# Optimization experiments

Hardware: AMD Instinct MI355X
Metric: run time of the kernel (lower is better)

The kernel has to match this reference:

```python
import jax, jax.numpy as jnp
import numpy as np

N_NODES = 1_000_000
N_EDGES = 16_000_000


def setup_inputs() -> dict:
    key = jax.random.key(0)
    k_feat, k_norm, k_src, k_dst, k_w1, k_w2 = jax.random.split(key, 6)
    feat = jax.random.normal(k_feat, (N_NODES, 1), dtype=jnp.float32)
    norm = jax.random.uniform(k_norm, (N_NODES, 1), dtype=jnp.float32)
    src = jax.random.randint(k_src, (N_EDGES,), 0, N_NODES, dtype=jnp.int64 if jax.config.read('jax_enable_x64') else jnp.int32)
    dst = jax.random.randint(k_dst, (N_EDGES,), 0, N_NODES, dtype=jnp.int64 if jax.config.read('jax_enable_x64') else jnp.int32)
    # GCNLayer1: in_feats=1 -> out_feats=3; GCNLayer2: 3 -> 1 (hardcoded in GCNProtein)
    W1 = jax.random.normal(k_w1, (1, 3), dtype=jnp.float32) * (1.0 / np.sqrt(1.0))
    b1 = jnp.zeros((3,), dtype=jnp.float32)
    W2 = jax.random.normal(k_w2, (3, 1), dtype=jnp.float32) * (1.0 / np.sqrt(3.0))
    b2 = jnp.zeros((1,), dtype=jnp.float32)
    return {"feat": feat, "norm": norm, "src": src, "dst": dst,
            "W1": W1, "b1": b1, "W2": W2, "b2": b2}


def gcn_layer(src, dst, x, norm, W, b):
    # symmetric-normalized GCN message passing (DGL GraphConv semantics):
    # h = norm * x ; h = sum_{(u->v) in E} h[u] scattered to v ; h = norm * h ; h = h @ W + b ; relu
    h = x * norm                                   # [N, F]
    msgs = jnp.take(h, src, axis=0)                # [E, F] gather (irregular)
    agg = jax.ops.segment_sum(msgs, dst, num_segments=x.shape[0])  # [N, F] scatter-add
    h = agg * norm                                 # [N, F]
    h = h @ W + b                                  # tiny GEMM: F_in -> F_out
    return jax.nn.relu(h)


def reference(feat, norm, src, dst, W1, b1, W2, b2):
    h = gcn_layer(src, dst, feat, norm, W1, b1)    # [N, 3]
    h = gcn_layer(src, dst, h, norm, W2, b2)       # [N, 1]
    return h
```

## Files before the change

kernel.cpp:

```cpp
#include <hip/hip_runtime.h>

#define BSHIFT 10
#define BSZ (1 << BSHIFT)
#define NBMAX 1024
#define NBIN_BLOCKS 1024
#define PB 512
#define BATCH 8192


__global__ void k1b(const float* __restrict__ feat, const float* __restrict__ norm,
                    float* __restrict__ g1, int n) {
    int stride = gridDim.x * blockDim.x;
    for (int i = blockIdx.x * blockDim.x + threadIdx.x; i < n; i += stride)
        g1[i] = feat[i] * norm[i];
}

__global__ void k1_prep(const float* __restrict__ feat, const float* __restrict__ norm,
                        float* __restrict__ g1, float* __restrict__ agg1,
                        float* __restrict__ agg2, int n) {
    int stride = gridDim.x * blockDim.x;
    for (int i = blockIdx.x * blockDim.x + threadIdx.x; i < n; i += stride) {
        g1[i] = feat[i] * norm[i];
        agg1[i] = 0.0f;
        agg2[i] = 0.0f;
    }
}

__global__ void k3_mid(const float* __restrict__ agg1, const float* __restrict__ norm,
                       const float* __restrict__ W1, const float* __restrict__ b1,
                       const float* __restrict__ W2, float* __restrict__ t, int n) {
    float w10 = W1[0], w11 = W1[1], w12 = W1[2];
    float b10 = b1[0], b11 = b1[1], b12 = b1[2];
    float w20 = W2[0], w21 = W2[1], w22 = W2[2];
    int stride = gridDim.x * blockDim.x;
    for (int i = blockIdx.x * blockDim.x + threadIdx.x; i < n; i += stride) {
        float nv = norm[i];
        float s = agg1[i] * nv;
        float h0 = fmaxf(fmaf(s, w10, b10), 0.0f);
        float h1 = fmaxf(fmaf(s, w11, b11), 0.0f);
        float h2 = fmaxf(fmaf(s, w12, b12), 0.0f);
        t[i] = nv * (h0 * w20 + h1 * w21 + h2 * w22);
    }
}

__global__ void k5_out(const float* __restrict__ agg2, const float* __restrict__ norm,
                       const float* __restrict__ b2, float* __restrict__ out, int n) {
    float b = b2[0];
    int stride = gridDim.x * blockDim.x;
    for (int i = blockIdx.x * blockDim.x + threadIdx.x; i < n; i += stride)
        out[i] = fmaxf(agg2[i] * norm[i] + b, 0.0f);
}


__global__ void k_hist(const int* __restrict__ dst, int nE, int NB, int chunk,
                       int* __restrict__ counts) {
    extern __shared__ int lhist[];
    int t = threadIdx.x;
    for (int b = t; b < NB; b += blockDim.x) lhist[b] = 0;
    __syncthreads();
    int lo = blockIdx.x * chunk;
    int hi = min(lo + chunk, nE);
    int n4 = (hi - lo) >> 2;
    const int4* d4 = (const int4*)(dst + lo);
    for (int i = t; i < n4; i += blockDim.x) {
        int4 v = d4[i];
        atomicAdd(&lhist[v.x >> BSHIFT], 1);
        atomicAdd(&lhist[v.y >> BSHIFT], 1);
        atomicAdd(&lhist[v.z >> BSHIFT], 1);
        atomicAdd(&lhist[v.w >> BSHIFT], 1);
    }
    for (int i = lo + (n4 << 2) + t; i < hi; i += blockDim.x)
        atomicAdd(&lhist[dst[i] >> BSHIFT], 1);
    __syncthreads();
    for (int b = t; b < NB; b += blockDim.x)
        counts[(size_t)b * NBIN_BLOCKS + blockIdx.x] = lhist[b];
}

__global__ void k_bucketscan(const int* __restrict__ counts,
                             int* __restrict__ chunkpre, int* __restrict__ tot) {
    __shared__ int ssum[256];
    int b = blockIdx.x;
    int t = threadIdx.x;
    const int4* in4 = (const int4*)(counts + (size_t)b * NBIN_BLOCKS);
    int4 v = in4[t];
    int mysum = v.x + v.y + v.z + v.w;
    ssum[t] = mysum;
    __syncthreads();
    for (int ofs = 1; ofs < 256; ofs <<= 1) {
        int add = (t >= ofs) ? ssum[t - ofs] : 0;
        __syncthreads();
        ssum[t] += add;
        __syncthreads();
    }
    int excl = ssum[t] - mysum;
    int4 o;
    o.x = excl;
    o.y = excl + v.x;
    o.z = o.y + v.y;
    o.w = o.z + v.z;
    ((int4*)(chunkpre + (size_t)b * NBIN_BLOCKS))[t] = o;
    if (t == 255) tot[b] = ssum[255];
}

__global__ void k_exscan(const int* __restrict__ tot, int NB, int* __restrict__ base) {
    __shared__ int s[1024];
    int t = threadIdx.x;
    if (NB < 1024) {
        int v = (t < NB) ? tot[t] : 0;
        s[t] = v;
        __syncthreads();
        for (int ofs = 1; ofs < 1024; ofs <<= 1) {
            int add = (t >= ofs) ? s[t - ofs] : 0;
            __syncthreads();
            s[t] += add;
            __syncthreads();
        }
        if (t < NB) base[t] = s[t] - v;
        if (t == NB) base[NB] = s[NB - 1];
    } else if (t == 0) {
        int run = 0;
        for (int b = 0; b < NB; ++b) { base[b] = run; run += tot[b]; }
        base[NB] = run;
    }
}

__global__ void __launch_bounds__(PB)
k_place2(const int* __restrict__ src, const int* __restrict__ dst,
         int nE, int NB, int chunk,
         const int* __restrict__ chunkpre, const int* __restrict__ base,
         unsigned int* __restrict__ bpack) {
    __shared__ unsigned int spack[BATCH];
    __shared__ unsigned short sbkt[BATCH];
    __shared__ int lcur[NBMAX];
    __shared__ int loff[NBMAX + 1];
    __shared__ int gcur[NBMAX];
    __shared__ int ssc[PB];
    int t = threadIdx.x;
    int blk = blockIdx.x;

    for (int b = t; b < NB; b += PB)
        gcur[b] = base[b] + chunkpre[(size_t)b * NBIN_BLOCKS + blk];

    int lo = blk * chunk;
    int hi = min(lo + chunk, nE);
    for (int bs = lo; bs < hi; bs += BATCH) {
        int be = min(bs + BATCH, hi);
        int cnt = be - bs;
        lcur[2 * t] = 0;
        lcur[2 * t + 1] = 0;
        __syncthreads();
        int n4 = cnt >> 2;
        const int4* d4 = (const int4*)(dst + bs);
        for (int i = t; i < n4; i += PB) {
            int4 v = d4[i];
            atomicAdd(&lcur[v.x >> BSHIFT], 1);
            atomicAdd(&lcur[v.y >> BSHIFT], 1);
            atomicAdd(&lcur[v.z >> BSHIFT], 1);
            atomicAdd(&lcur[v.w >> BSHIFT], 1);
        }
        for (int i = bs + (n4 << 2) + t; i < be; i += PB)
            atomicAdd(&lcur[dst[i] >> BSHIFT], 1);
        __syncthreads();
        int a = lcur[2 * t];
        int c = lcur[2 * t + 1];
        int s = a + c;
        ssc[t] = s;
        __syncthreads();
        for (int ofs = 1; ofs < PB; ofs <<= 1) {
            int add = (t >= ofs) ? ssc[t - ofs] : 0;
            __syncthreads();
            ssc[t] += add;
            __syncthreads();
        }
        int excl = ssc[t] - s;
        loff[2 * t] = excl;
        loff[2 * t + 1] = excl + a;
        lcur[2 * t] = excl;
        lcur[2 * t + 1] = excl + a;
        if (t == PB - 1) loff[2 * PB] = ssc[PB - 1];
        __syncthreads();
        const int4* s4 = (const int4*)(src + bs);
        for (int i = t; i < n4; i += PB) {
            int4 dv = d4[i];
            int4 sv = s4[i];
            int b0 = dv.x >> BSHIFT, p0 = atomicAdd(&lcur[b0], 1);
            spack[p0] = ((unsigned int)sv.x << BSHIFT) | (unsigned int)(dv.x & (BSZ - 1));
            sbkt[p0] = (unsigned short)b0;
            int b1 = dv.y >> BSHIFT, p1 = atomicAdd(&lcur[b1], 1);
            spack[p1] = ((unsigned int)sv.y << BSHIFT) | (unsigned int)(dv.y & (BSZ - 1));
            sbkt[p1] = (unsigned short)b1;
            int b2 = dv.z >> BSHIFT, p2 = atomicAdd(&lcur[b2], 1);
            spack[p2] = ((unsigned int)sv.z << BSHIFT) | (unsigned int)(dv.z & (BSZ - 1));
            sbkt[p2] = (unsigned short)b2;
            int b3 = dv.w >> BSHIFT, p3 = atomicAdd(&lcur[b3], 1);
            spack[p3] = ((unsigned int)sv.w << BSHIFT) | (unsigned int)(dv.w & (BSZ - 1));
            sbkt[p3] = (unsigned short)b3;
        }
        for (int i = bs + (n4 << 2) + t; i < be; i += PB) {
            int d = dst[i];
            int b = d >> BSHIFT;
            int pos = atomicAdd(&lcur[b], 1);
            spack[pos] = ((unsigned int)src[i] << BSHIFT) | (unsigned int)(d & (BSZ - 1));
            sbkt[pos] = (unsigned short)b;
        }
        __syncthreads();
        for (int j = t; j < cnt; j += PB) {
            int b = sbkt[j];
            bpack[gcur[b] + (j - loff[b])] = spack[j];
        }
        __syncthreads();
        for (int b = t; b < NB; b += PB)
            gcur[b] += loff[b + 1] - loff[b];
        __syncthreads();
    }
}

__device__ __forceinline__ void acc_body(const unsigned int* __restrict__ bpack,
                                         int lo, int hi,
                                         const float* __restrict__ val,
                                         float* acc) {
    int head = min((4 - (lo & 3)) & 3, hi - lo);
    for (int i = lo + (int)threadIdx.x; i < lo + head; i += blockDim.x) {
        unsigned int w = bpack[i];
        atomicAdd(&acc[w & (BSZ - 1)], val[w >> BSHIFT]);
    }
    int lo4 = lo + head;
    int n4 = (hi - lo4) >> 2;
    const uint4* p4 = (const uint4*)(bpack + lo4);
    int i = threadIdx.x;
    int bd = blockDim.x;
    for (; i + bd < n4; i += 2 * bd) {
        uint4 wa = p4[i];
        uint4 wb = p4[i + bd];
        float va0 = val[wa.x >> BSHIFT], va1 = val[wa.y >> BSHIFT];
        float va2 = val[wa.z >> BSHIFT], va3 = val[wa.w >> BSHIFT];
        float vb0 = val[wb.x >> BSHIFT], vb1 = val[wb.y >> BSHIFT];
        float vb2 = val[wb.z >> BSHIFT], vb3 = val[wb.w >> BSHIFT];
        atomicAdd(&acc[wa.x & (BSZ - 1)], va0);
        atomicAdd(&acc[wa.y & (BSZ - 1)], va1);
        atomicAdd(&acc[wa.z & (BSZ - 1)], va2);
        atomicAdd(&acc[wa.w & (BSZ - 1)], va3);
        atomicAdd(&acc[wb.x & (BSZ - 1)], vb0);
        atomicAdd(&acc[wb.y & (BSZ - 1)], vb1);
        atomicAdd(&acc[wb.z & (BSZ - 1)], vb2);
        atomicAdd(&acc[wb.w & (BSZ - 1)], vb3);
    }
    for (; i < n4; i += bd) {
        uint4 w = p4[i];
        atomicAdd(&acc[w.x & (BSZ - 1)], val[w.x >> BSHIFT]);
        atomicAdd(&acc[w.y & (BSZ - 1)], val[w.y >> BSHIFT]);
        atomicAdd(&acc[w.z & (BSZ - 1)], val[w.z >> BSHIFT]);
        atomicAdd(&acc[w.w & (BSZ - 1)], val[w.w >> BSHIFT]);
    }
    for (int j = lo4 + (n4 << 2) + (int)threadIdx.x; j < hi; j += blockDim.x) {
        unsigned int w = bpack[j];
        atomicAdd(&acc[w & (BSZ - 1)], val[w >> BSHIFT]);
    }
}

__global__ void k_acc1(const unsigned int* __restrict__ bpack,
                       const int* __restrict__ base,
                       const float* __restrict__ val, const float* __restrict__ norm,
                       const float* __restrict__ W1, const float* __restrict__ b1,
                       const float* __restrict__ W2,
                       float* __restrict__ t, int nN) {
    __shared__ float acc[BSZ];
    for (int j = threadIdx.x; j < BSZ; j += blockDim.x) acc[j] = 0.0f;
    __syncthreads();
    int b = blockIdx.x;
    acc_body(bpack, base[b], base[b + 1], val, acc);
    __syncthreads();
    float w10 = W1[0], w11 = W1[1], w12 = W1[2];
    float b10 = b1[0], b11 = b1[1], b12 = b1[2];
    float w20 = W2[0], w21 = W2[1], w22 = W2[2];
    int node0 = b << BSHIFT;
    for (int j = threadIdx.x; j < BSZ && node0 + j < nN; j += blockDim.x) {
        float nv = norm[node0 + j];
        float s = acc[j] * nv;
        float h0 = fmaxf(fmaf(s, w10, b10), 0.0f);
        float h1 = fmaxf(fmaf(s, w11, b11), 0.0f);
        float h2 = fmaxf(fmaf(s, w12, b12), 0.0f);
        t[node0 + j] = nv * (h0 * w20 + h1 * w21 + h2 * w22);
    }
}

__global__ void k_acc2(const unsigned int* __restrict__ bpack,
                       const int* __restrict__ base,
                       const float* __restrict__ val, const float* __restrict__ norm,
                       const float* __restrict__ b2,
                       float* __restrict__ out, int nN) {
    __shared__ float acc[BSZ];
    for (int j = threadIdx.x; j < BSZ; j += blockDim.x) acc[j] = 0.0f;
    __syncthreads();
    int b = blockIdx.x;
    acc_body(bpack, base[b], base[b + 1], val, acc);
    __syncthreads();
    float bb = b2[0];
    int node0 = b << BSHIFT;
    for (int j = threadIdx.x; j < BSZ && node0 + j < nN; j += blockDim.x)
        out[node0 + j] = fmaxf(acc[j] * norm[node0 + j] + bb, 0.0f);
}

__global__ void k_edge_scatter(const int* __restrict__ src, const int* __restrict__ dst,
                               const float* __restrict__ val, float* __restrict__ agg,
                               int nE) {
    int stride = gridDim.x * blockDim.x;
    for (int e = blockIdx.x * blockDim.x + threadIdx.x; e < nE; e += stride)
        atomicAdd(&agg[dst[e]], val[src[e]]);
}

static inline size_t align256(size_t x) { return (x + 255) & ~(size_t)255; }

extern "C" void kernel_launch(void* const* d_in, const int* in_sizes, int n_in,
                              void* d_out, int out_size, void* d_ws, size_t ws_size,
                              hipStream_t stream) {
    const float* feat = (const float*)d_in[0];
    const float* norm = (const float*)d_in[1];
    const int*   src  = (const int*)d_in[2];
    const int*   dst  = (const int*)d_in[3];
    const float* W1   = (const float*)d_in[4];
    const float* b1   = (const float*)d_in[5];
    const float* W2   = (const float*)d_in[6];
    const float* b2   = (const float*)d_in[7];
    float* out = (float*)d_out;

    int nN = in_sizes[0];
    int nE = in_sizes[2];
    int NB = (nN + BSZ - 1) >> BSHIFT;

    char* p = (char*)d_ws;
    size_t off = 0;
    float* g1   = (float*)(p + off); off = align256(off + (size_t)nN * 4);
    float* agg1 = (float*)(p + off); off = align256(off + (size_t)nN * 4);
    int* base     = (int*)(p + off); off = align256(off + (size_t)(NB + 1) * 4);
    int* tot      = (int*)(p + off); off = align256(off + (size_t)NB * 4);
    float* agg2   = (float*)(p + off);
    int* counts   = (int*)(p + off); off = align256(off + (size_t)NB * NBIN_BLOCKS * 4);
    int* chunkpre = (int*)(p + off); off = align256(off + (size_t)NB * NBIN_BLOCKS * 4);
    unsigned int* bpack = (unsigned int*)(p + off); off = align256(off + (size_t)nE * 4);
    size_t need = off;

    const int BLK = 256;
    int nodeBlocks = (nN + BLK - 1) / BLK;
    if (nodeBlocks > 2048) nodeBlocks = 2048;

    bool packed_ok = ((size_t)nN <= ((size_t)1 << (32 - BSHIFT))) && (NB <= NBMAX);
    if (ws_size >= need && packed_ok) {
        int chunk = (nE + NBIN_BLOCKS - 1) / NBIN_BLOCKS;
        chunk = (chunk + 3) & ~3;
        size_t ldsNB = (size_t)NB * 4;

        k1b<<<nodeBlocks, BLK, 0, stream>>>(feat, norm, g1, nN);
        k_hist<<<NBIN_BLOCKS, 256, ldsNB, stream>>>(dst, nE, NB, chunk, counts);
        k_bucketscan<<<NB, 256, 0, stream>>>(counts, chunkpre, tot);
        k_exscan<<<1, 1024, 0, stream>>>(tot, NB, base);
        k_place2<<<NBIN_BLOCKS, PB, 0, stream>>>(src, dst, nE, NB, chunk,
                                                 chunkpre, base, bpack);
        k_acc1<<<NB, 512, 0, stream>>>(bpack, base, g1, norm, W1, b1, W2, agg1, nN);
        k_acc2<<<NB, 512, 0, stream>>>(bpack, base, agg1, norm, b2, out, nN);
    } else {
        int edgeBlocks = 2048;
        k1_prep<<<nodeBlocks, BLK, 0, stream>>>(feat, norm, g1, agg1, agg2, nN);
        k_edge_scatter<<<edgeBlocks, BLK, 0, stream>>>(src, dst, g1, agg1, nE);
        k3_mid<<<nodeBlocks, BLK, 0, stream>>>(agg1, norm, W1, b1, W2, g1, nN);
        k_edge_scatter<<<edgeBlocks, BLK, 0, stream>>>(src, dst, g1, agg2, nE);
        k5_out<<<nodeBlocks, BLK, 0, stream>>>(agg2, norm, b2, out, nN);
    }
}
```

Before: 282.7 us.

## Widen dst buckets to 2048 nodes and split each bucket across two blocks

Doubles the bucket width so there are about 489 buckets, which simplifies the per-batch scan in the placement kernel to one bucket per thread. Each bucket's edge range is then split between two accumulation blocks that write partial sums to global memory, and separate merge kernels add the two halves and apply the norm, weights and relu. This keeps the number of accumulation blocks near the old count while halving per-block LDS atomic contention ranges. The cost is extra global traffic for the partials, two more kernel launches, and twice the LDS accumulator per block. The histogram block size also grows to 512.

```diff
diff --git a/kernel.cpp b/kernel.cpp
--- a/kernel.cpp
+++ b/kernel.cpp
@@ -1,8 +1,8 @@
 #include <hip/hip_runtime.h>
 
-#define BSHIFT 10
+#define BSHIFT 11
 #define BSZ (1 << BSHIFT)
-#define NBMAX 1024
+#define NBMAX 512
 #define NBIN_BLOCKS 1024
 #define PB 512
 #define BATCH 8192
@@ -134,7 +134,7 @@
     __shared__ int lcur[NBMAX];
     __shared__ int loff[NBMAX + 1];
     __shared__ int gcur[NBMAX];
-    __shared__ int ssc[PB];
+    __shared__ int ssc[NBMAX];
     int t = threadIdx.x;
     int blk = blockIdx.x;
 
@@ -146,8 +146,7 @@
     for (int bs = lo; bs < hi; bs += BATCH) {
         int be = min(bs + BATCH, hi);
         int cnt = be - bs;
-        lcur[2 * t] = 0;
-        lcur[2 * t + 1] = 0;
+        lcur[t] = 0;
         __syncthreads();
         int n4 = cnt >> 2;
         const int4* d4 = (const int4*)(dst + bs);
@@ -161,23 +160,19 @@
         for (int i = bs + (n4 << 2) + t; i < be; i += PB)
             atomicAdd(&lcur[dst[i] >> BSHIFT], 1);
         __syncthreads();
-        int a = lcur[2 * t];
-        int c = lcur[2 * t + 1];
-        int s = a + c;
-        ssc[t] = s;
-        __syncthreads();
-        for (int ofs = 1; ofs < PB; ofs <<= 1) {
+        int v = lcur[t];
+        ssc[t] = v;
+        __syncthreads();
+        for (int ofs = 1; ofs < 512; ofs <<= 1) {
             int add = (t >= ofs) ? ssc[t - ofs] : 0;
             __syncthreads();
             ssc[t] += add;
             __syncthreads();
         }
-        int excl = ssc[t] - s;
-        loff[2 * t] = excl;
-        loff[2 * t + 1] = excl + a;
-        lcur[2 * t] = excl;
-        lcur[2 * t + 1] = excl + a;
-        if (t == PB - 1) loff[2 * PB] = ssc[PB - 1];
+        int excl = ssc[t] - v;
+        loff[t] = excl;
+        lcur[t] = excl;
+        if (t == 511) loff[512] = ssc[511];
         __syncthreads();
         const int4* s4 = (const int4*)(src + bs);
         for (int i = t; i < n4; i += PB) {
@@ -258,47 +253,64 @@
     }
 }
 
-__global__ void k_acc1(const unsigned int* __restrict__ bpack,
+__global__ void k_accp(const unsigned int* __restrict__ bpack,
                        const int* __restrict__ base,
-                       const float* __restrict__ val, const float* __restrict__ norm,
-                       const float* __restrict__ W1, const float* __restrict__ b1,
-                       const float* __restrict__ W2,
-                       float* __restrict__ t, int nN) {
+                       const float* __restrict__ val,
+                       float* __restrict__ partial, int nN) {
     __shared__ float acc[BSZ];
     for (int j = threadIdx.x; j < BSZ; j += blockDim.x) acc[j] = 0.0f;
     __syncthreads();
-    int b = blockIdx.x;
-    acc_body(bpack, base[b], base[b + 1], val, acc);
-    __syncthreads();
+    int bid = blockIdx.x;
+    int b = bid >> 1;
+    int s = bid & 1;
+    int lo = base[b], hi = base[b + 1];
+    int mid = (lo + hi) >> 1;
+    int rlo = s ? mid : lo;
+    int rhi = s ? hi : mid;
+    acc_body(bpack, rlo, rhi, val, acc);
+    __syncthreads();
+    float* dstp = partial + (size_t)s * nN;
+    int node0 = b << BSHIFT;
+    int lim = min(BSZ, nN - node0);
+    int l4 = lim >> 2;
+    float4* d4 = (float4*)(dstp + node0);
+    const float4* a4 = (const float4*)acc;
+    for (int j = threadIdx.x; j < l4; j += blockDim.x) d4[j] = a4[j];
+    for (int j = (l4 << 2) + (int)threadIdx.x; j < lim; j += blockDim.x)
+        dstp[node0 + j] = acc[j];
+}
+
+__global__ void k_merge1(const float* __restrict__ partial,
+                         const float* __restrict__ norm,
+                         const float* __restrict__ W1, const float* __restrict__ b1,
+                         const float* __restrict__ W2,
+                         float* __restrict__ t, int nN) {
     float w10 = W1[0], w11 = W1[1], w12 = W1[2];
     float b10 = b1[0], b11 = b1[1], b12 = b1[2];
     float w20 = W2[0], w21 = W2[1], w22 = W2[2];
-    int node0 = b << BSHIFT;
-    for (int j = threadIdx.x; j < BSZ && node0 + j < nN; j += blockDim.x) {
-        float nv = norm[node0 + j];
-        float s = acc[j] * nv;
+    const float* p0 = partial;
+    const float* p1 = partial + nN;
+    int stride = gridDim.x * blockDim.x;
+    for (int i = blockIdx.x * blockDim.x + threadIdx.x; i < nN; i += stride) {
+        float nv = norm[i];
+        float s = (p0[i] + p1[i]) * nv;
         float h0 = fmaxf(fmaf(s, w10, b10), 0.0f);
         float h1 = fmaxf(fmaf(s, w11, b11), 0.0f);
         float h2 = fmaxf(fmaf(s, w12, b12), 0.0f);
-        t[node0 + j] = nv * (h0 * w20 + h1 * w21 + h2 * w22);
-    }
-}
-
-__global__ void k_acc2(const unsigned int* __restrict__ bpack,
-                       const int* __restrict__ base,
-                       const float* __restrict__ val, const float* __restrict__ norm,
-                       const float* __restrict__ b2,
-                       float* __restrict__ out, int nN) {
-    __shared__ float acc[BSZ];
-    for (int j = threadIdx.x; j < BSZ; j += blockDim.x) acc[j] = 0.0f;
-    __syncthreads();
-    int b = blockIdx.x;
-    acc_body(bpack, base[b], base[b + 1], val, acc);
-    __syncthreads();
+        t[i] = nv * (h0 * w20 + h1 * w21 + h2 * w22);
+    }
+}
+
+__global__ void k_merge2(const float* __restrict__ partial,
+                         const float* __restrict__ norm,
+                         const float* __restrict__ b2,
+                         float* __restrict__ out, int nN) {
     float bb = b2[0];
-    int node0 = b << BSHIFT;
-    for (int j = threadIdx.x; j < BSZ && node0 + j < nN; j += blockDim.x)
-        out[node0 + j] = fmaxf(acc[j] * norm[node0 + j] + bb, 0.0f);
+    const float* p0 = partial;
+    const float* p1 = partial + nN;
+    int stride = gridDim.x * blockDim.x;
+    for (int i = blockIdx.x * blockDim.x + threadIdx.x; i < nN; i += stride)
+        out[i] = fmaxf((p0[i] + p1[i]) * norm[i] + bb, 0.0f);
 }
 
 __global__ void k_edge_scatter(const int* __restrict__ src, const int* __restrict__ dst,
@@ -332,6 +344,7 @@
     size_t off = 0;
     float* g1   = (float*)(p + off); off = align256(off + (size_t)nN * 4);
     float* agg1 = (float*)(p + off); off = align256(off + (size_t)nN * 4);
+    float* partial = (float*)(p + off); off = align256(off + 2 * (size_t)nN * 4);
     int* base     = (int*)(p + off); off = align256(off + (size_t)(NB + 1) * 4);
     int* tot      = (int*)(p + off); off = align256(off + (size_t)NB * 4);
     float* agg2   = (float*)(p + off);
@@ -351,13 +364,15 @@
         size_t ldsNB = (size_t)NB * 4;
 
         k1b<<<nodeBlocks, BLK, 0, stream>>>(feat, norm, g1, nN);
-        k_hist<<<NBIN_BLOCKS, 256, ldsNB, stream>>>(dst, nE, NB, chunk, counts);
+        k_hist<<<NBIN_BLOCKS, 512, ldsNB, stream>>>(dst, nE, NB, chunk, counts);
         k_bucketscan<<<NB, 256, 0, stream>>>(counts, chunkpre, tot);
         k_exscan<<<1, 1024, 0, stream>>>(tot, NB, base);
         k_place2<<<NBIN_BLOCKS, PB, 0, stream>>>(src, dst, nE, NB, chunk,
                                                  chunkpre, base, bpack);
-        k_acc1<<<NB, 512, 0, stream>>>(bpack, base, g1, norm, W1, b1, W2, agg1, nN);
-        k_acc2<<<NB, 512, 0, stream>>>(bpack, base, agg1, norm, b2, out, nN);
+        k_accp<<<2 * NB, 512, 0, stream>>>(bpack, base, g1, partial, nN);
+        k_merge1<<<nodeBlocks, BLK, 0, stream>>>(partial, norm, W1, b1, W2, agg1, nN);
+        k_accp<<<2 * NB, 512, 0, stream>>>(bpack, base, agg1, partial, nN);
+        k_merge2<<<nodeBlocks, BLK, 0, stream>>>(partial, norm, b2, out, nN);
     } else {
         int edgeBlocks = 2048;
         k1_prep<<<nodeBlocks, BLK, 0, stream>>>(feat, norm, g1, agg1, agg2, nN);
```

Result: faster. 274.6 us (-2.9%).

## Embed first-layer gathered values in bucketed edge records and widen buckets

Applied to the files above, without the earlier changes.

During the bucket-placement pass, each edge record now also carries g1[src], stored as an 8-byte (packed index, value) pair. The first accumulation kernel can then read values in a streaming fashion instead of doing random gathers. The bucket width doubles to 2048 nodes, so there are half as many bucket blocks, and loads and stores of the bucket array use nontemporal hints. The cost is twice the bpack write and read traffic, plus the random gather moving into the placement kernel. The second layer still gathers from the 8-byte records, reading unused value slots.

```diff
diff --git a/kernel.cpp b/kernel.cpp
--- a/kernel.cpp
+++ b/kernel.cpp
@@ -1,11 +1,15 @@
 #include <hip/hip_runtime.h>
 
-#define BSHIFT 10
+#define BSHIFT 11
 #define BSZ (1 << BSHIFT)
-#define NBMAX 1024
+#define NBMAX 512
 #define NBIN_BLOCKS 1024
 #define PB 512
 #define BATCH 8192
+
+typedef int          int32x4  __attribute__((ext_vector_type(4)));
+typedef unsigned int uint32x4 __attribute__((ext_vector_type(4)));
+typedef unsigned int uint32x2 __attribute__((ext_vector_type(2)));
 
 
 __global__ void k1b(const float* __restrict__ feat, const float* __restrict__ norm,
@@ -124,17 +128,18 @@
     }
 }
 
+template <bool IV>
 __global__ void __launch_bounds__(PB)
-k_place2(const int* __restrict__ src, const int* __restrict__ dst,
-         int nE, int NB, int chunk,
-         const int* __restrict__ chunkpre, const int* __restrict__ base,
-         unsigned int* __restrict__ bpack) {
+k_place2x(const int* __restrict__ src, const int* __restrict__ dst,
+          const float* __restrict__ g1, int nE, int NB, int chunk,
+          const int* __restrict__ chunkpre, const int* __restrict__ base,
+          unsigned int* __restrict__ bpack, uint32x2* __restrict__ bpack2) {
     __shared__ unsigned int spack[BATCH];
     __shared__ unsigned short sbkt[BATCH];
     __shared__ int lcur[NBMAX];
     __shared__ int loff[NBMAX + 1];
     __shared__ int gcur[NBMAX];
-    __shared__ int ssc[PB];
+    __shared__ int ssc[NBMAX];
     int t = threadIdx.x;
     int blk = blockIdx.x;
 
@@ -146,8 +151,7 @@
     for (int bs = lo; bs < hi; bs += BATCH) {
         int be = min(bs + BATCH, hi);
         int cnt = be - bs;
-        lcur[2 * t] = 0;
-        lcur[2 * t + 1] = 0;
+        lcur[t] = 0;
         __syncthreads();
         int n4 = cnt >> 2;
         const int4* d4 = (const int4*)(dst + bs);
@@ -161,23 +165,19 @@
         for (int i = bs + (n4 << 2) + t; i < be; i += PB)
             atomicAdd(&lcur[dst[i] >> BSHIFT], 1);
         __syncthreads();
-        int a = lcur[2 * t];
-        int c = lcur[2 * t + 1];
-        int s = a + c;
-        ssc[t] = s;
-        __syncthreads();
-        for (int ofs = 1; ofs < PB; ofs <<= 1) {
+        int v = lcur[t];
+        ssc[t] = v;
+        __syncthreads();
+        for (int ofs = 1; ofs < 512; ofs <<= 1) {
             int add = (t >= ofs) ? ssc[t - ofs] : 0;
             __syncthreads();
             ssc[t] += add;
             __syncthreads();
         }
-        int excl = ssc[t] - s;
-        loff[2 * t] = excl;
-        loff[2 * t + 1] = excl + a;
-        lcur[2 * t] = excl;
-        lcur[2 * t + 1] = excl + a;
-        if (t == PB - 1) loff[2 * PB] = ssc[PB - 1];
+        int excl = ssc[t] - v;
+        loff[t] = excl;
+        lcur[t] = excl;
+        if (t == 511) loff[512] = ssc[511];
         __syncthreads();
         const int4* s4 = (const int4*)(src + bs);
         for (int i = t; i < n4; i += PB) {
@@ -205,8 +205,18 @@
         }
         __syncthreads();
         for (int j = t; j < cnt; j += PB) {
+            unsigned int w = spack[j];
             int b = sbkt[j];
-            bpack[gcur[b] + (j - loff[b])] = spack[j];
+            int gi = gcur[b] + (j - loff[b]);
+            if (IV) {
+                float vv = g1[w >> BSHIFT];
+                uint32x2 o;
+                o[0] = w;
+                o[1] = __float_as_uint(vv);
+                __builtin_nontemporal_store(o, bpack2 + gi);
+            } else {
+                __builtin_nontemporal_store(w, bpack + gi);
+            }
         }
         __syncthreads();
         for (int b = t; b < NB; b += PB)
@@ -214,6 +224,105 @@
         __syncthreads();
     }
 }
+
+
+__global__ void k_acc1v2(const uint32x2* __restrict__ bp, const int* __restrict__ base,
+                         const float* __restrict__ norm,
+                         const float* __restrict__ W1, const float* __restrict__ b1,
+                         const float* __restrict__ W2,
+                         float* __restrict__ t, int nN) {
+    __shared__ float acc[BSZ];
+    for (int j = threadIdx.x; j < BSZ; j += blockDim.x) acc[j] = 0.0f;
+    __syncthreads();
+    int b = blockIdx.x;
+    int lo = base[b], hi = base[b + 1];
+    int head = ((lo & 1) && lo < hi) ? 1 : 0;
+    if (head && threadIdx.x == 0) {
+        uint32x2 w = bp[lo];
+        atomicAdd(&acc[w[0] & (BSZ - 1)], __uint_as_float(w[1]));
+    }
+    int lo2 = lo + head;
+    int n2 = (hi - lo2) >> 1;
+    const uint32x4* p4 = (const uint32x4*)(bp + lo2);
+    int i = threadIdx.x, bd = blockDim.x;
+    for (; i + bd < n2; i += 2 * bd) {
+        uint32x4 a = __builtin_nontemporal_load(p4 + i);
+        uint32x4 c = __builtin_nontemporal_load(p4 + i + bd);
+        atomicAdd(&acc[a[0] & (BSZ - 1)], __uint_as_float(a[1]));
+        atomicAdd(&acc[a[2] & (BSZ - 1)], __uint_as_float(a[3]));
+        atomicAdd(&acc[c[0] & (BSZ - 1)], __uint_as_float(c[1]));
+        atomicAdd(&acc[c[2] & (BSZ - 1)], __uint_as_float(c[3]));
+    }
+    for (; i < n2; i += bd) {
+        uint32x4 a = __builtin_nontemporal_load(p4 + i);
+        atomicAdd(&acc[a[0] & (BSZ - 1)], __uint_as_float(a[1]));
+        atomicAdd(&acc[a[2] & (BSZ - 1)], __uint_as_float(a[3]));
+    }
+    for (int j = lo2 + (n2 << 1) + (int)threadIdx.x; j < hi; j += bd) {
+        uint32x2 w = bp[j];
+        atomicAdd(&acc[w[0] & (BSZ - 1)], __uint_as_float(w[1]));
+    }
+    __syncthreads();
+    float w10 = W1[0], w11 = W1[1], w12 = W1[2];
+    float b10 = b1[0], b11 = b1[1], b12 = b1[2];
+    float w20 = W2[0], w21 = W2[1], w22 = W2[2];
+    int node0 = b << BSHIFT;
+    for (int j = threadIdx.x; j < BSZ && node0 + j < nN; j += blockDim.x) {
+        float nv = norm[node0 + j];
+        float s = acc[j] * nv;
+        float h0 = fmaxf(fmaf(s, w10, b10), 0.0f);
+        float h1 = fmaxf(fmaf(s, w11, b11), 0.0f);
+        float h2 = fmaxf(fmaf(s, w12, b12), 0.0f);
+        t[node0 + j] = nv * (h0 * w20 + h1 * w21 + h2 * w22);
+    }
+}
+
+__global__ void k_acc2v2(const uint32x2* __restrict__ bp, const int* __restrict__ base,
+                         const float* __restrict__ val, const float* __restrict__ norm,
+                         const float* __restrict__ b2,
+                         float* __restrict__ out, int nN) {
+    __shared__ float acc[BSZ];
+    for (int j = threadIdx.x; j < BSZ; j += blockDim.x) acc[j] = 0.0f;
+    __syncthreads();
+    int b = blockIdx.x;
+    int lo = base[b], hi = base[b + 1];
+    int head = ((lo & 1) && lo < hi) ? 1 : 0;
+    if (head && threadIdx.x == 0) {
+        uint32x2 w = bp[lo];
+        atomicAdd(&acc[w[0] & (BSZ - 1)], val[w[0] >> BSHIFT]);
+    }
+    int lo2 = lo + head;
+    int n2 = (hi - lo2) >> 1;
+    const uint32x4* p4 = (const uint32x4*)(bp + lo2);
+    int i = threadIdx.x, bd = blockDim.x;
+    for (; i + bd < n2; i += 2 * bd) {
+        uint32x4 a = __builtin_nontemporal_load(p4 + i);
+        uint32x4 c = __builtin_nontemporal_load(p4 + i + bd);
+        float v0 = val[a[0] >> BSHIFT];
+        float v1 = val[a[2] >> BSHIFT];
+        float v2 = val[c[0] >> BSHIFT];
+        float v3 = val[c[2] >> BSHIFT];
+        atomicAdd(&acc[a[0] & (BSZ - 1)], v0);
+        atomicAdd(&acc[a[2] & (BSZ - 1)], v1);
+        atomicAdd(&acc[c[0] & (BSZ - 1)], v2);
+        atomicAdd(&acc[c[2] & (BSZ - 1)], v3);
+    }
+    for (; i < n2; i += bd) {
+        uint32x4 a = __builtin_nontemporal_load(p4 + i);
+        atomicAdd(&acc[a[0] & (BSZ - 1)], val[a[0] >> BSHIFT]);
+        atomicAdd(&acc[a[2] & (BSZ - 1)], val[a[2] >> BSHIFT]);
+    }
+    for (int j = lo2 + (n2 << 1) + (int)threadIdx.x; j < hi; j += bd) {
+        uint32x2 w = bp[j];
+        atomicAdd(&acc[w[0] & (BSZ - 1)], val[w[0] >> BSHIFT]);
+    }
+    __syncthreads();
+    float bb = b2[0];
+    int node0 = b << BSHIFT;
+    for (int j = threadIdx.x; j < BSZ && node0 + j < nN; j += blockDim.x)
+        out[node0 + j] = fmaxf(acc[j] * norm[node0 + j] + bb, 0.0f);
+}
+
 
 __device__ __forceinline__ void acc_body(const unsigned int* __restrict__ bpack,
                                          int lo, int hi,
@@ -226,31 +335,31 @@
     }
     int lo4 = lo + head;
     int n4 = (hi - lo4) >> 2;
-    const uint4* p4 = (const uint4*)(bpack + lo4);
+    const uint32x4* p4 = (const uint32x4*)(bpack + lo4);
     int i = threadIdx.x;
     int bd = blockDim.x;
     for (; i + bd < n4; i += 2 * bd) {
-        uint4 wa = p4[i];
-        uint4 wb = p4[i + bd];
-        float va0 = val[wa.x >> BSHIFT], va1 = val[wa.y >> BSHIFT];
-        float va2 = val[wa.z >> BSHIFT], va3 = val[wa.w >> BSHIFT];
-        float vb0 = val[wb.x >> BSHIFT], vb1 = val[wb.y >> BSHIFT];
-        float vb2 = val[wb.z >> BSHIFT], vb3 = val[wb.w >> BSHIFT];
-        atomicAdd(&acc[wa.x & (BSZ - 1)], va0);
-        atomicAdd(&acc[wa.y & (BSZ - 1)], va1);
-        atomicAdd(&acc[wa.z & (BSZ - 1)], va2);
-        atomicAdd(&acc[wa.w & (BSZ - 1)], va3);
-        atomicAdd(&acc[wb.x & (BSZ - 1)], vb0);
-        atomicAdd(&acc[wb.y & (BSZ - 1)], vb1);
-        atomicAdd(&acc[wb.z & (BSZ - 1)], vb2);
-        atomicAdd(&acc[wb.w & (BSZ - 1)], vb3);
+        uint32x4 wa = __builtin_nontemporal_load(p4 + i);
+        uint32x4 wb = __builtin_nontemporal_load(p4 + i + bd);
+        float va0 = val[wa[0] >> BSHIFT], va1 = val[wa[1] >> BSHIFT];
+        float va2 = val[wa[2] >> BSHIFT], va3 = val[wa[3] >> BSHIFT];
+        float vb0 = val[wb[0] >> BSHIFT], vb1 = val[wb[1] >> BSHIFT];
+        float vb2 = val[wb[2] >> BSHIFT], vb3 = val[wb[3] >> BSHIFT];
+        atomicAdd(&acc[wa[0] & (BSZ - 1)], va0);
+        atomicAdd(&acc[wa[1] & (BSZ - 1)], va1);
+        atomicAdd(&acc[wa[2] & (BSZ - 1)], va2);
+        atomicAdd(&acc[wa[3] & (BSZ - 1)], va3);
+        atomicAdd(&acc[wb[0] & (BSZ - 1)], vb0);
+        atomicAdd(&acc[wb[1] & (BSZ - 1)], vb1);
+        atomicAdd(&acc[wb[2] & (BSZ - 1)], vb2);
+        atomicAdd(&acc[wb[3] & (BSZ - 1)], vb3);
     }
     for (; i < n4; i += bd) {
-        uint4 w = p4[i];
-        atomicAdd(&acc[w.x & (BSZ - 1)], val[w.x >> BSHIFT]);
-        atomicAdd(&acc[w.y & (BSZ - 1)], val[w.y >> BSHIFT]);
-        atomicAdd(&acc[w.z & (BSZ - 1)], val[w.z >> BSHIFT]);
-        atomicAdd(&acc[w.w & (BSZ - 1)], val[w.w >> BSHIFT]);
+        uint32x4 w = __builtin_nontemporal_load(p4 + i);
+        atomicAdd(&acc[w[0] & (BSZ - 1)], val[w[0] >> BSHIFT]);
+        atomicAdd(&acc[w[1] & (BSZ - 1)], val[w[1] >> BSHIFT]);
+        atomicAdd(&acc[w[2] & (BSZ - 1)], val[w[2] >> BSHIFT]);
+        atomicAdd(&acc[w[3] & (BSZ - 1)], val[w[3] >> BSHIFT]);
     }
     for (int j = lo4 + (n4 << 2) + (int)threadIdx.x; j < hi; j += blockDim.x) {
         unsigned int w = bpack[j];
@@ -330,39 +439,50 @@
 
     char* p = (char*)d_ws;
     size_t off = 0;
-    float* g1   = (float*)(p + off); off = align256(off + (size_t)nN * 4);
-    float* agg1 = (float*)(p + off); off = align256(off + (size_t)nN * 4);
+    float* g1 = (float*)(p + off); off = align256(off + (size_t)nN * 4);
+    float* t1 = (float*)(p + off); off = align256(off + (size_t)nN * 4);
     int* base     = (int*)(p + off); off = align256(off + (size_t)(NB + 1) * 4);
     int* tot      = (int*)(p + off); off = align256(off + (size_t)NB * 4);
     float* agg2   = (float*)(p + off);
     int* counts   = (int*)(p + off); off = align256(off + (size_t)NB * NBIN_BLOCKS * 4);
     int* chunkpre = (int*)(p + off); off = align256(off + (size_t)NB * NBIN_BLOCKS * 4);
-    unsigned int* bpack = (unsigned int*)(p + off); off = align256(off + (size_t)nE * 4);
-    size_t need = off;
+    size_t off_common = off;
+    uint32x2* bpack2 = (uint32x2*)(p + off_common);
+    unsigned int* bpack = (unsigned int*)(p + off_common);
+    size_t need2 = align256(off_common + (size_t)nE * 8);
+    size_t need1 = align256(off_common + (size_t)nE * 4);
 
     const int BLK = 256;
     int nodeBlocks = (nN + BLK - 1) / BLK;
     if (nodeBlocks > 2048) nodeBlocks = 2048;
 
     bool packed_ok = ((size_t)nN <= ((size_t)1 << (32 - BSHIFT))) && (NB <= NBMAX);
-    if (ws_size >= need && packed_ok) {
+    if (packed_ok && ws_size >= need1) {
         int chunk = (nE + NBIN_BLOCKS - 1) / NBIN_BLOCKS;
         chunk = (chunk + 3) & ~3;
         size_t ldsNB = (size_t)NB * 4;
+        bool v2 = (ws_size >= need2);
 
         k1b<<<nodeBlocks, BLK, 0, stream>>>(feat, norm, g1, nN);
-        k_hist<<<NBIN_BLOCKS, 256, ldsNB, stream>>>(dst, nE, NB, chunk, counts);
+        k_hist<<<NBIN_BLOCKS, 512, ldsNB, stream>>>(dst, nE, NB, chunk, counts);
         k_bucketscan<<<NB, 256, 0, stream>>>(counts, chunkpre, tot);
         k_exscan<<<1, 1024, 0, stream>>>(tot, NB, base);
-        k_place2<<<NBIN_BLOCKS, PB, 0, stream>>>(src, dst, nE, NB, chunk,
-                                                 chunkpre, base, bpack);
-        k_acc1<<<NB, 512, 0, stream>>>(bpack, base, g1, norm, W1, b1, W2, agg1, nN);
-        k_acc2<<<NB, 512, 0, stream>>>(bpack, base, agg1, norm, b2, out, nN);
+        if (v2) {
+            k_place2x<true><<<NBIN_BLOCKS, PB, 0, stream>>>(src, dst, g1, nE, NB, chunk,
+                                                            chunkpre, base, nullptr, bpack2);
+            k_acc1v2<<<NB, 512, 0, stream>>>(bpack2, base, norm, W1, b1, W2, t1, nN);
+            k_acc2v2<<<NB, 512, 0, stream>>>(bpack2, base, t1, norm, b2, out, nN);
+        } else {
+            k_place2x<false><<<NBIN_BLOCKS, PB, 0, stream>>>(src, dst, g1, nE, NB, chunk,
+                                                             chunkpre, base, bpack, nullptr);
+            k_acc1<<<NB, 512, 0, stream>>>(bpack, base, g1, norm, W1, b1, W2, t1, nN);
+            k_acc2<<<NB, 512, 0, stream>>>(bpack, base, t1, norm, b2, out, nN);
+        }
     } else {
         int edgeBlocks = 2048;
-        k1_prep<<<nodeBlocks, BLK, 0, stream>>>(feat, norm, g1, agg1, agg2, nN);
-        k_edge_scatter<<<edgeBlocks, BLK, 0, stream>>>(src, dst, g1, agg1, nE);
-        k3_mid<<<nodeBlocks, BLK, 0, stream>>>(agg1, norm, W1, b1, W2, g1, nN);
+        k1_prep<<<nodeBlocks, BLK, 0, stream>>>(feat, norm, g1, t1, agg2, nN);
+        k_edge_scatter<<<edgeBlocks, BLK, 0, stream>>>(src, dst, g1, t1, nE);
+        k3_mid<<<nodeBlocks, BLK, 0, stream>>>(t1, norm, W1, b1, W2, g1, nN);
         k_edge_scatter<<<edgeBlocks, BLK, 0, stream>>>(src, dst, g1, agg2, nE);
         k5_out<<<nodeBlocks, BLK, 0, stream>>>(agg2, norm, b2, out, nN);
     }
```

New measurement: 351.5 us. 1.24x slower.

## Widen buckets to 2048 nodes, keep edges in registers, use nontemporal loads

Applied to the files above, without the earlier changes.

Doubles the destination bucket width so there are about 489 buckets, one per thread in the placement scan. The placement kernel now loads each batch's src/dst once into registers and reuses them for both the count and scatter passes instead of reading dst twice. The accumulation loads packed edges with nontemporal hints, and the histogram kernel uses 512 threads. Each accumulation block now holds 2048 shared accumulators and covers more edges, so there are fewer, larger blocks. The register-cached path assumes a batch holds at most 4*PB int4s, which BATCH=8192 satisfies.

```diff
diff --git a/kernel.cpp b/kernel.cpp
--- a/kernel.cpp
+++ b/kernel.cpp
@@ -1,11 +1,13 @@
 #include <hip/hip_runtime.h>
 
-#define BSHIFT 10
+#define BSHIFT 11
 #define BSZ (1 << BSHIFT)
-#define NBMAX 1024
+#define NBMAX 512
 #define NBIN_BLOCKS 1024
 #define PB 512
 #define BATCH 8192
+
+typedef unsigned int uint32x4 __attribute__((ext_vector_type(4)));
 
 
 __global__ void k1b(const float* __restrict__ feat, const float* __restrict__ norm,
@@ -134,7 +136,7 @@
     __shared__ int lcur[NBMAX];
     __shared__ int loff[NBMAX + 1];
     __shared__ int gcur[NBMAX];
-    __shared__ int ssc[PB];
+    __shared__ int ssc[NBMAX];
     int t = threadIdx.x;
     int blk = blockIdx.x;
 
@@ -146,55 +148,61 @@
     for (int bs = lo; bs < hi; bs += BATCH) {
         int be = min(bs + BATCH, hi);
         int cnt = be - bs;
-        lcur[2 * t] = 0;
-        lcur[2 * t + 1] = 0;
+        lcur[t] = 0;
         __syncthreads();
         int n4 = cnt >> 2;
         const int4* d4 = (const int4*)(dst + bs);
-        for (int i = t; i < n4; i += PB) {
-            int4 v = d4[i];
-            atomicAdd(&lcur[v.x >> BSHIFT], 1);
-            atomicAdd(&lcur[v.y >> BSHIFT], 1);
-            atomicAdd(&lcur[v.z >> BSHIFT], 1);
-            atomicAdd(&lcur[v.w >> BSHIFT], 1);
+        const int4* s4 = (const int4*)(src + bs);
+        int4 dvs[4], svs[4];
+        #pragma unroll
+        for (int u = 0; u < 4; ++u) {
+            int i = t + u * PB;
+            if (i < n4) {
+                int4 dv = d4[i];
+                int4 sv = s4[i];
+                dvs[u] = dv; svs[u] = sv;
+                atomicAdd(&lcur[dv.x >> BSHIFT], 1);
+                atomicAdd(&lcur[dv.y >> BSHIFT], 1);
+                atomicAdd(&lcur[dv.z >> BSHIFT], 1);
+                atomicAdd(&lcur[dv.w >> BSHIFT], 1);
+            }
         }
         for (int i = bs + (n4 << 2) + t; i < be; i += PB)
             atomicAdd(&lcur[dst[i] >> BSHIFT], 1);
         __syncthreads();
-        int a = lcur[2 * t];
-        int c = lcur[2 * t + 1];
-        int s = a + c;
-        ssc[t] = s;
-        __syncthreads();
-        for (int ofs = 1; ofs < PB; ofs <<= 1) {
+        int v = lcur[t];
+        ssc[t] = v;
+        __syncthreads();
+        for (int ofs = 1; ofs < 512; ofs <<= 1) {
             int add = (t >= ofs) ? ssc[t - ofs] : 0;
             __syncthreads();
             ssc[t] += add;
             __syncthreads();
         }
-        int excl = ssc[t] - s;
-        loff[2 * t] = excl;
-        loff[2 * t + 1] = excl + a;
-        lcur[2 * t] = excl;
-        lcur[2 * t + 1] = excl + a;
-        if (t == PB - 1) loff[2 * PB] = ssc[PB - 1];
-        __syncthreads();
-        const int4* s4 = (const int4*)(src + bs);
-        for (int i = t; i < n4; i += PB) {
-            int4 dv = d4[i];
-            int4 sv = s4[i];
-            int b0 = dv.x >> BSHIFT, p0 = atomicAdd(&lcur[b0], 1);
-            spack[p0] = ((unsigned int)sv.x << BSHIFT) | (unsigned int)(dv.x & (BSZ - 1));
-            sbkt[p0] = (unsigned short)b0;
-            int b1 = dv.y >> BSHIFT, p1 = atomicAdd(&lcur[b1], 1);
-            spack[p1] = ((unsigned int)sv.y << BSHIFT) | (unsigned int)(dv.y & (BSZ - 1));
-            sbkt[p1] = (unsigned short)b1;
-            int b2 = dv.z >> BSHIFT, p2 = atomicAdd(&lcur[b2], 1);
-            spack[p2] = ((unsigned int)sv.z << BSHIFT) | (unsigned int)(dv.z & (BSZ - 1));
-            sbkt[p2] = (unsigned short)b2;
-            int b3 = dv.w >> BSHIFT, p3 = atomicAdd(&lcur[b3], 1);
-            spack[p3] = ((unsigned int)sv.w << BSHIFT) | (unsigned int)(dv.w & (BSZ - 1));
-            sbkt[p3] = (unsigned short)b3;
+        int excl = ssc[t] - v;
+        loff[t] = excl;
+        lcur[t] = excl;
+        if (t == 511) loff[512] = ssc[511];
+        __syncthreads();
+        #pragma unroll
+        for (int u = 0; u < 4; ++u) {
+            int i = t + u * PB;
+            if (i < n4) {
+                int4 dv = dvs[u];
+                int4 sv = svs[u];
+                int b0 = dv.x >> BSHIFT, p0 = atomicAdd(&lcur[b0], 1);
+                spack[p0] = ((unsigned int)sv.x << BSHIFT) | (unsigned int)(dv.x & (BSZ - 1));
+                sbkt[p0] = (unsigned short)b0;
+                int b1 = dv.y >> BSHIFT, p1 = atomicAdd(&lcur[b1], 1);
+                spack[p1] = ((unsigned int)sv.y << BSHIFT) | (unsigned int)(dv.y & (BSZ - 1));
+                sbkt[p1] = (unsigned short)b1;
+                int b2 = dv.z >> BSHIFT, p2 = atomicAdd(&lcur[b2], 1);
+                spack[p2] = ((unsigned int)sv.z << BSHIFT) | (unsigned int)(dv.z & (BSZ - 1));
+                sbkt[p2] = (unsigned short)b2;
+                int b3 = dv.w >> BSHIFT, p3 = atomicAdd(&lcur[b3], 1);
+                spack[p3] = ((unsigned int)sv.w << BSHIFT) | (unsigned int)(dv.w & (BSZ - 1));
+                sbkt[p3] = (unsigned short)b3;
+            }
         }
         for (int i = bs + (n4 << 2) + t; i < be; i += PB) {
             int d = dst[i];
@@ -226,31 +234,31 @@
     }
     int lo4 = lo + head;
     int n4 = (hi - lo4) >> 2;
-    const uint4* p4 = (const uint4*)(bpack + lo4);
+    const uint32x4* p4 = (const uint32x4*)(bpack + lo4);
     int i = threadIdx.x;
     int bd = blockDim.x;
     for (; i + bd < n4; i += 2 * bd) {
-        uint4 wa = p4[i];
-        uint4 wb = p4[i + bd];
-        float va0 = val[wa.x >> BSHIFT], va1 = val[wa.y >> BSHIFT];
-        float va2 = val[wa.z >> BSHIFT], va3 = val[wa.w >> BSHIFT];
-        float vb0 = val[wb.x >> BSHIFT], vb1 = val[wb.y >> BSHIFT];
-        float vb2 = val[wb.z >> BSHIFT], vb3 = val[wb.w >> BSHIFT];
-        atomicAdd(&acc[wa.x & (BSZ - 1)], va0);
-        atomicAdd(&acc[wa.y & (BSZ - 1)], va1);
-        atomicAdd(&acc[wa.z & (BSZ - 1)], va2);
-        atomicAdd(&acc[wa.w & (BSZ - 1)], va3);
-        atomicAdd(&acc[wb.x & (BSZ - 1)], vb0);
-        atomicAdd(&acc[wb.y & (BSZ - 1)], vb1);
-        atomicAdd(&acc[wb.z & (BSZ - 1)], vb2);
-        atomicAdd(&acc[wb.w & (BSZ - 1)], vb3);
+        uint32x4 wa = __builtin_nontemporal_load(p4 + i);
+        uint32x4 wb = __builtin_nontemporal_load(p4 + i + bd);
+        float va0 = val[wa[0] >> BSHIFT], va1 = val[wa[1] >> BSHIFT];
+        float va2 = val[wa[2] >> BSHIFT], va3 = val[wa[3] >> BSHIFT];
+        float vb0 = val[wb[0] >> BSHIFT], vb1 = val[wb[1] >> BSHIFT];
+        float vb2 = val[wb[2] >> BSHIFT], vb3 = val[wb[3] >> BSHIFT];
+        atomicAdd(&acc[wa[0] & (BSZ - 1)], va0);
+        atomicAdd(&acc[wa[1] & (BSZ - 1)], va1);
+        atomicAdd(&acc[wa[2] & (BSZ - 1)], va2);
+        atomicAdd(&acc[wa[3] & (BSZ - 1)], va3);
+        atomicAdd(&acc[wb[0] & (BSZ - 1)], vb0);
+        atomicAdd(&acc[wb[1] & (BSZ - 1)], vb1);
+        atomicAdd(&acc[wb[2] & (BSZ - 1)], vb2);
+        atomicAdd(&acc[wb[3] & (BSZ - 1)], vb3);
     }
     for (; i < n4; i += bd) {
-        uint4 w = p4[i];
-        atomicAdd(&acc[w.x & (BSZ - 1)], val[w.x >> BSHIFT]);
-        atomicAdd(&acc[w.y & (BSZ - 1)], val[w.y >> BSHIFT]);
-        atomicAdd(&acc[w.z & (BSZ - 1)], val[w.z >> BSHIFT]);
-        atomicAdd(&acc[w.w & (BSZ - 1)], val[w.w >> BSHIFT]);
+        uint32x4 w = __builtin_nontemporal_load(p4 + i);
+        atomicAdd(&acc[w[0] & (BSZ - 1)], val[w[0] >> BSHIFT]);
+        atomicAdd(&acc[w[1] & (BSZ - 1)], val[w[1] >> BSHIFT]);
+        atomicAdd(&acc[w[2] & (BSZ - 1)], val[w[2] >> BSHIFT]);
+        atomicAdd(&acc[w[3] & (BSZ - 1)], val[w[3] >> BSHIFT]);
     }
     for (int j = lo4 + (n4 << 2) + (int)threadIdx.x; j < hi; j += blockDim.x) {
         unsigned int w = bpack[j];
@@ -330,8 +338,8 @@
 
     char* p = (char*)d_ws;
     size_t off = 0;
-    float* g1   = (float*)(p + off); off = align256(off + (size_t)nN * 4);
-    float* agg1 = (float*)(p + off); off = align256(off + (size_t)nN * 4);
+    float* g1 = (float*)(p + off); off = align256(off + (size_t)nN * 4);
+    float* t1 = (float*)(p + off); off = align256(off + (size_t)nN * 4);
     int* base     = (int*)(p + off); off = align256(off + (size_t)(NB + 1) * 4);
     int* tot      = (int*)(p + off); off = align256(off + (size_t)NB * 4);
     float* agg2   = (float*)(p + off);
@@ -345,24 +353,24 @@
     if (nodeBlocks > 2048) nodeBlocks = 2048;
 
     bool packed_ok = ((size_t)nN <= ((size_t)1 << (32 - BSHIFT))) && (NB <= NBMAX);
-    if (ws_size >= need && packed_ok) {
+    if (packed_ok && ws_size >= need) {
         int chunk = (nE + NBIN_BLOCKS - 1) / NBIN_BLOCKS;
         chunk = (chunk + 3) & ~3;
         size_t ldsNB = (size_t)NB * 4;
 
         k1b<<<nodeBlocks, BLK, 0, stream>>>(feat, norm, g1, nN);
-        k_hist<<<NBIN_BLOCKS, 256, ldsNB, stream>>>(dst, nE, NB, chunk, counts);
+        k_hist<<<NBIN_BLOCKS, 512, ldsNB, stream>>>(dst, nE, NB, chunk, counts);
         k_bucketscan<<<NB, 256, 0, stream>>>(counts, chunkpre, tot);
         k_exscan<<<1, 1024, 0, stream>>>(tot, NB, base);
         k_place2<<<NBIN_BLOCKS, PB, 0, stream>>>(src, dst, nE, NB, chunk,
                                                  chunkpre, base, bpack);
-        k_acc1<<<NB, 512, 0, stream>>>(bpack, base, g1, norm, W1, b1, W2, agg1, nN);
-        k_acc2<<<NB, 512, 0, stream>>>(bpack, base, agg1, norm, b2, out, nN);
+        k_acc1<<<NB, 512, 0, stream>>>(bpack, base, g1, norm, W1, b1, W2, t1, nN);
+        k_acc2<<<NB, 512, 0, stream>>>(bpack, base, t1, norm, b2, out, nN);
     } else {
         int edgeBlocks = 2048;
-        k1_prep<<<nodeBlocks, BLK, 0, stream>>>(feat, norm, g1, agg1, agg2, nN);
-        k_edge_scatter<<<edgeBlocks, BLK, 0, stream>>>(src, dst, g1, agg1, nE);
-        k3_mid<<<nodeBlocks, BLK, 0, stream>>>(agg1, norm, W1, b1, W2, g1, nN);
+        k1_prep<<<nodeBlocks, BLK, 0, stream>>>(feat, norm, g1, t1, agg2, nN);
+        k_edge_scatter<<<edgeBlocks, BLK, 0, stream>>>(src, dst, g1, t1, nE);
+        k3_mid<<<nodeBlocks, BLK, 0, stream>>>(t1, norm, W1, b1, W2, g1, nN);
         k_edge_scatter<<<edgeBlocks, BLK, 0, stream>>>(src, dst, g1, agg2, nE);
         k5_out<<<nodeBlocks, BLK, 0, stream>>>(agg2, norm, b2, out, nN);
     }
```

Measured after the change: 270.4 us. 4.3% less time.
